# Optimization experiments

Measured on AMD Instinct MI355X. Metric: run time of the kernel, lower is better.

## Reference

```python
import jax, jax.numpy as jnp
import numpy as np

EPS = 1e-5
HEADS = 4
DIM_HEAD = 64


def setup_inputs() -> dict:
    key = jax.random.key(0)
    k1, k2, k3, k4, k5, k6 = jax.random.split(key, 6)
    B, C, T, H, W = 2, 128, 40, 8, 8
    inner = HEADS * DIM_HEAD  # 256
    x = jax.random.normal(k1, (B, C, T, H, W), dtype=jnp.float32)
    g = jnp.ones((1, C, 1, 1, 1), dtype=jnp.float32) + 0.1 * jax.random.normal(k2, (1, C, 1, 1, 1), dtype=jnp.float32)
    b = 0.1 * jax.random.normal(k3, (1, C, 1, 1, 1), dtype=jnp.float32)
    w_qkv = 0.02 * jax.random.normal(k4, (inner * 3, C), dtype=jnp.float32)  # Conv1d(dim, inner*3, 1) weight squeezed
    w_out = 0.02 * jax.random.normal(k5, (C, inner), dtype=jnp.float32)      # Conv1d(inner, dim, 1) weight squeezed
    b_out = 0.02 * jax.random.normal(k6, (C,), dtype=jnp.float32)
    return {"x": x, "g": g, "b": b, "w_qkv": w_qkv, "w_out": w_out, "b_out": b_out}


def reference(x, g, b, w_qkv, w_out, b_out):
    B, C, T, H, W = x.shape
    n = T * H * W
    scale = DIM_HEAD ** -0.5
    # channel LayerNorm (var over dim=1, unbiased=False)
    mean = jnp.mean(x, axis=1, keepdims=True)
    std = jnp.sqrt(jnp.var(x, axis=1, keepdims=True))
    xn = (x - mean) / (std + EPS) * g + b
    xf = xn.reshape(B, C, n)  # b c n
    # 1x1 conv == matmul over channels
    qkv = jnp.einsum('oc,bcn->bon', w_qkv, xf)
    q, k, v = jnp.split(qkv, 3, axis=1)  # each [B, heads*d, n]
    def to_heads(t):  # b (h d) n -> b h n d
        return t.reshape(B, HEADS, DIM_HEAD, n).transpose(0, 1, 3, 2)
    q, k, v = to_heads(q) * scale, to_heads(k), to_heads(v)
    sim = jnp.einsum('bhid,bhjd->bhij', q, k)
    attn = jax.nn.softmax(sim, axis=-1)
    out = jnp.einsum('bhij,bhjd->bhid', attn, v)
    out = out.transpose(0, 1, 3, 2).reshape(B, HEADS * DIM_HEAD, n)  # b (h d) n
    out = jnp.einsum('oc,bcn->bon', w_out, out) + b_out[None, :, None]
    return out.reshape(B, C, T, H, W)
```

## Files before the change

kernel.cpp:

```cpp
#include <hip/hip_runtime.h>
#include <hip/hip_bf16.h>

#define HEADS 4
#define DHEAD 64
#define CC 128
#define NPOS 2560
#define NB 2

#define XN_ELE  ((size_t)NB * NPOS * CC)
#define QKV_ELE ((size_t)NB * HEADS * NPOS * DHEAD)
#define WS_TOTAL (XN_ELE + 4 * QKV_ELE)

typedef __attribute__((ext_vector_type(8))) short short8;
typedef __attribute__((ext_vector_type(4))) short short4_t;
typedef __attribute__((ext_vector_type(4))) float f32x4;

#define SIDX(row, col) (((row) << 6) + ((col) ^ (((row) & 7) << 3)))

static __device__ __forceinline__ float b2f(short u) {
    union { unsigned int i; float f; } v;
    v.i = ((unsigned int)(unsigned short)u) << 16;
    return v.f;
}
static __device__ __forceinline__ short f2b(float f) {
    __hip_bfloat16 h = __float2bfloat16(f);
    union { __hip_bfloat16 h; unsigned short u; } v; v.h = h;
    return (short)v.u;
}

__global__ __launch_bounds__(256) void ln_kernel(
    const float* __restrict__ x, const float* __restrict__ g,
    const float* __restrict__ bb, short* __restrict__ xn) {
    int p0 = blockIdx.x * 64, b = blockIdx.y;
    __shared__ float tile[128][65];
    __shared__ float redsum[4][64], redsq[4][64], meanS[64], invS[64];
    int t = threadIdx.x, p = t & 63, cpart = t >> 6;
    float s = 0.f, sq = 0.f;
    for (int k = 0; k < 32; k++) {
        int c = cpart * 32 + k;
        float v = x[((b * CC + c) * NPOS) + p0 + p];
        tile[c][p] = v;
        s += v; sq += v * v;
    }
    redsum[cpart][p] = s; redsq[cpart][p] = sq;
    __syncthreads();
    if (t < 64) {
        float S = redsum[0][t] + redsum[1][t] + redsum[2][t] + redsum[3][t];
        float Q = redsq[0][t] + redsq[1][t] + redsq[2][t] + redsq[3][t];
        float mean = S * (1.f / CC);
        float var = fmaxf(Q * (1.f / CC) - mean * mean, 0.f);
        meanS[t] = mean;
        invS[t] = 1.f / (sqrtf(var) + 1e-5f);
    }
    __syncthreads();
    for (int k = 0; k < 32; k++) {
        int idx = k * 256 + t;
        int c = idx & 127, pp = idx >> 7;
        float v = (tile[c][pp] - meanS[pp]) * invS[pp] * g[c] + bb[c];
        xn[((size_t)(b * NPOS) + p0 + pp) * CC + c] = f2b(v);
    }
}

__global__ __launch_bounds__(256) void qkv_kernel(
    const float* __restrict__ w, const short* __restrict__ xn,
    short* __restrict__ q_ws, short* __restrict__ k_ws, short* __restrict__ v_ws) {
    int pt = blockIdx.x, ot = blockIdx.y, b = blockIdx.z;
    int p0 = pt * 64, o0 = ot * 64;
    __shared__ short Ws[64][136];
    __shared__ short Xs[64][136];
    int t = threadIdx.x, wv = t >> 6, l = t & 63;
    for (int i = 0; i < 8; i++) {
        int gidx = i * 256 + t;
        int r = gidx >> 5, cg = gidx & 31;
        f32x4 wv4 = *(const f32x4*)&w[(size_t)(o0 + r) * CC + cg * 4];
        short4_t sv = { f2b(wv4[0]), f2b(wv4[1]), f2b(wv4[2]), f2b(wv4[3]) };
        *(short4_t*)&Ws[r][cg * 4] = sv;
    }
    for (int i = 0; i < 4; i++) {
        int idx = i * 256 + t;
        int r = idx >> 4, ch = idx & 15;
        *(short8*)&Xs[r][ch * 8] = *(const short8*)&xn[((size_t)(b * NPOS) + p0 + r) * CC + ch * 8];
    }
    __syncthreads();
    f32x4 acc[4] = {{0,0,0,0},{0,0,0,0},{0,0,0,0},{0,0,0,0}};
    int lr = l & 15, lg = l >> 4;
    for (int kk = 0; kk < 4; kk++) {
        short8 a = *(short8*)&Ws[wv * 16 + lr][kk * 32 + lg * 8];
        for (int fb = 0; fb < 4; fb++) {
            short8 bf = *(short8*)&Xs[fb * 16 + lr][kk * 32 + lg * 8];
            acc[fb] = __builtin_amdgcn_mfma_f32_16x16x32_bf16(a, bf, acc[fb], 0, 0, 0);
        }
    }
    int orow0 = o0 + wv * 16 + lg * 4;
    int sec = orow0 >> 8;
    int oi = orow0 & 255, h = oi >> 6, d0 = oi & 63;
    size_t bh = (size_t)(b * HEADS + h);
    for (int fb = 0; fb < 4; fb++) {
        int pos = p0 + fb * 16 + lr;
        if (sec == 0) {
            short4_t qv = { f2b(acc[fb][0] * 0.125f), f2b(acc[fb][1] * 0.125f),
                            f2b(acc[fb][2] * 0.125f), f2b(acc[fb][3] * 0.125f) };
            *(short4_t*)&q_ws[(bh * NPOS + pos) * DHEAD + d0] = qv;
        } else if (sec == 1) {
            short4_t kv = { f2b(acc[fb][0]), f2b(acc[fb][1]), f2b(acc[fb][2]), f2b(acc[fb][3]) };
            *(short4_t*)&k_ws[(bh * NPOS + pos) * DHEAD + d0] = kv;
        } else {
            for (int r = 0; r < 4; r++)
                v_ws[(bh * DHEAD + d0 + r) * NPOS + pos] = f2b(acc[fb][r]);
        }
    }
}

__global__ __launch_bounds__(256) void attn_kernel(
    const short* __restrict__ q_ws, const short* __restrict__ k_ws,
    const short* __restrict__ v_ws, short* __restrict__ o_ws) {
    int qt = blockIdx.x, bh = blockIdx.y;
    int q0 = qt * 64;
    __shared__ short Ks[2][64 * 64];
    __shared__ short Vs[2][64 * 64];
    __shared__ short PsT[64 * 64];
    int t = threadIdx.x, wv = t >> 6, l = t & 63;
    int lr = l & 15, lg = l >> 4;
    int sr0 = t >> 3, sr1 = sr0 + 32, sc = (t & 7) * 8;
    const short* kbp = k_ws + (size_t)bh * NPOS * DHEAD;
    const short* vbp = v_ws + (size_t)bh * DHEAD * NPOS;

    short8 qreg[2];
    for (int kk = 0; kk < 2; kk++)
        qreg[kk] = *(const short8*)&q_ws[((size_t)bh * NPOS + q0 + wv * 16 + lr) * DHEAD + kk * 32 + lg * 8];

    *(short8*)&Ks[0][SIDX(sr0, sc)] = *(const short8*)&kbp[(size_t)sr0 * DHEAD + sc];
    *(short8*)&Ks[0][SIDX(sr1, sc)] = *(const short8*)&kbp[(size_t)sr1 * DHEAD + sc];
    *(short8*)&Vs[0][SIDX(sr0, sc)] = *(const short8*)&vbp[(size_t)sr0 * NPOS + sc];
    *(short8*)&Vs[0][SIDX(sr1, sc)] = *(const short8*)&vbp[(size_t)sr1 * NPOS + sc];
    __syncthreads();

    float m_ = -1e9f, l_ = 0.f;
    f32x4 acc[4] = {{0,0,0,0},{0,0,0,0},{0,0,0,0},{0,0,0,0}};
    int prow = wv * 16 + lr;

    for (int kt = 0; kt < NPOS / 64; kt++) {
        int cur = kt & 1;
        bool pf = (kt + 1 < NPOS / 64);
        short8 kr0, kr1, vr0, vr1;
        if (pf) {
            int koff = (kt + 1) * 64;
            kr0 = *(const short8*)&kbp[(size_t)(koff + sr0) * DHEAD + sc];
            kr1 = *(const short8*)&kbp[(size_t)(koff + sr1) * DHEAD + sc];
            vr0 = *(const short8*)&vbp[(size_t)sr0 * NPOS + koff + sc];
            vr1 = *(const short8*)&vbp[(size_t)sr1 * NPOS + koff + sc];
        }
        f32x4 sf[4] = {{0,0,0,0},{0,0,0,0},{0,0,0,0},{0,0,0,0}};
        #pragma unroll
        for (int kk = 0; kk < 2; kk++) {
            #pragma unroll
            for (int fb = 0; fb < 4; fb++) {
                short8 kb = *(short8*)&Ks[cur][SIDX(fb * 16 + lr, kk * 32 + lg * 8)];
                sf[fb] = __builtin_amdgcn_mfma_f32_16x16x32_bf16(kb, qreg[kk], sf[fb], 0, 0, 0);
            }
        }
        float m0 = fmaxf(fmaxf(sf[0][0], sf[0][1]), fmaxf(sf[0][2], sf[0][3]));
        float m1 = fmaxf(fmaxf(sf[1][0], sf[1][1]), fmaxf(sf[1][2], sf[1][3]));
        float m2 = fmaxf(fmaxf(sf[2][0], sf[2][1]), fmaxf(sf[2][2], sf[2][3]));
        float m3 = fmaxf(fmaxf(sf[3][0], sf[3][1]), fmaxf(sf[3][2], sf[3][3]));
        float mx = fmaxf(fmaxf(m0, m1), fmaxf(m2, m3));
        mx = fmaxf(mx, __shfl_xor(mx, 16, 64));
        mx = fmaxf(mx, __shfl_xor(mx, 32, 64));
        float nm = fmaxf(m_, mx);
        float alpha = __expf(m_ - nm);
        float ps[4][4];
        float rs = 0.f;
        #pragma unroll
        for (int fb = 0; fb < 4; fb++) {
            float s0 = __expf(sf[fb][0] - nm), s1 = __expf(sf[fb][1] - nm);
            float s2 = __expf(sf[fb][2] - nm), s3 = __expf(sf[fb][3] - nm);
            ps[fb][0] = s0; ps[fb][1] = s1; ps[fb][2] = s2; ps[fb][3] = s3;
            rs += (s0 + s1) + (s2 + s3);
        }
        rs += __shfl_xor(rs, 16, 64);
        rs += __shfl_xor(rs, 32, 64);
        l_ = l_ * alpha + rs;
        m_ = nm;
        #pragma unroll
        for (int db = 0; db < 4; db++) {
            acc[db][0] *= alpha; acc[db][1] *= alpha;
            acc[db][2] *= alpha; acc[db][3] *= alpha;
        }
        #pragma unroll
        for (int fb = 0; fb < 4; fb++) {
            short4_t pk = { f2b(ps[fb][0]), f2b(ps[fb][1]), f2b(ps[fb][2]), f2b(ps[fb][3]) };
            *(short4_t*)&PsT[SIDX(prow, fb * 16 + lg * 4)] = pk;
        }
        #pragma unroll
        for (int kk = 0; kk < 2; kk++) {
            short8 pb = *(short8*)&PsT[SIDX(prow, kk * 32 + lg * 8)];
            #pragma unroll
            for (int db = 0; db < 4; db++) {
                short8 va = *(short8*)&Vs[cur][SIDX(db * 16 + lr, kk * 32 + lg * 8)];
                acc[db] = __builtin_amdgcn_mfma_f32_16x16x32_bf16(va, pb, acc[db], 0, 0, 0);
            }
        }
        if (pf) {
            *(short8*)&Ks[cur ^ 1][SIDX(sr0, sc)] = kr0;
            *(short8*)&Ks[cur ^ 1][SIDX(sr1, sc)] = kr1;
            *(short8*)&Vs[cur ^ 1][SIDX(sr0, sc)] = vr0;
            *(short8*)&Vs[cur ^ 1][SIDX(sr1, sc)] = vr1;
        }
        __syncthreads();
    }

    int h = bh & (HEADS - 1), b = bh >> 2;
    float inv = 1.f / l_;
    int pos = q0 + prow;
    #pragma unroll
    for (int db = 0; db < 4; db++) {
        short4_t ov = { f2b(acc[db][0] * inv), f2b(acc[db][1] * inv),
                        f2b(acc[db][2] * inv), f2b(acc[db][3] * inv) };
        *(short4_t*)&o_ws[((size_t)(b * NPOS) + pos) * 256 + h * DHEAD + db * 16 + lg * 4] = ov;
    }
}

__global__ __launch_bounds__(256) void proj_kernel(
    const float* __restrict__ w_out, const float* __restrict__ b_out,
    const short* __restrict__ o_ws, float* __restrict__ out) {
    int pt = blockIdx.x, ct = blockIdx.y, b = blockIdx.z;
    int p0 = pt * 64, c0 = ct * 64;
    __shared__ short Ws[64][72];
    __shared__ short Os[64][72];
    int t = threadIdx.x, wv = t >> 6, l = t & 63;
    int lr = l & 15, lg = l >> 4;
    f32x4 acc[4] = {{0,0,0,0},{0,0,0,0},{0,0,0,0},{0,0,0,0}};
    for (int kc = 0; kc < 4; kc++) {
        __syncthreads();
        for (int i = 0; i < 4; i++) {
            int gidx = i * 256 + t;
            int r = gidx >> 4, cg = gidx & 15;
            f32x4 wv4 = *(const f32x4*)&w_out[(size_t)(c0 + r) * 256 + kc * 64 + cg * 4];
            short4_t sv = { f2b(wv4[0]), f2b(wv4[1]), f2b(wv4[2]), f2b(wv4[3]) };
            *(short4_t*)&Ws[r][cg * 4] = sv;
        }
        for (int i = 0; i < 2; i++) {
            int idx = i * 256 + t;
            int r = idx >> 3, ch = idx & 7;
            *(short8*)&Os[r][ch * 8] = *(const short8*)&o_ws[((size_t)(b * NPOS) + p0 + r) * 256 + kc * 64 + ch * 8];
        }
        __syncthreads();
        for (int kk = 0; kk < 2; kk++) {
            short8 a = *(short8*)&Ws[wv * 16 + lr][kk * 32 + lg * 8];
            for (int fb = 0; fb < 4; fb++) {
                short8 ob = *(short8*)&Os[fb * 16 + lr][kk * 32 + lg * 8];
                acc[fb] = __builtin_amdgcn_mfma_f32_16x16x32_bf16(a, ob, acc[fb], 0, 0, 0);
            }
        }
    }
    for (int r = 0; r < 4; r++) {
        int c = c0 + wv * 16 + lg * 4 + r;
        float bias = b_out[c];
        for (int fb = 0; fb < 4; fb++) {
            float vv = acc[fb][r] + bias;
            out[((size_t)(b * CC) + c) * NPOS + p0 + fb * 16 + lr] = vv;
        }
    }
}

extern "C" void kernel_launch(void* const* d_in, const int* in_sizes, int n_in,
                              void* d_out, int out_size, void* d_ws, size_t ws_size,
                              hipStream_t stream) {
    const float* x     = (const float*)d_in[0];
    const float* g     = (const float*)d_in[1];
    const float* b     = (const float*)d_in[2];
    const float* w_qkv = (const float*)d_in[3];
    const float* w_out = (const float*)d_in[4];
    const float* b_out = (const float*)d_in[5];
    float* out = (float*)d_out;

    const size_t out_bytes = (size_t)out_size * sizeof(float);
    const size_t ws_need   = WS_TOTAL * sizeof(short);

    {
        const int exp_sizes[6] = {655360, 128, 128, 98304, 32768, 128};
        int bad = -1;
        if (n_in != 6) bad = 15;
        else for (int i = 0; i < 6; i++) if (in_sizes[i] != exp_sizes[i]) { bad = i; break; }
        if (bad >= 0) { hipMemsetAsync(d_out, 0x50 | bad, out_bytes, stream); return; }
    }
    if (ws_size < ws_need) {
        int mb = (int)(ws_size >> 20); if (mb > 15) mb = 15;
        hipMemsetAsync(d_out, 0x40 | mb, out_bytes, stream);
        return;
    }

    short* xn   = (short*)d_ws;
    short* q_ws = xn + XN_ELE;
    short* k_ws = q_ws + QKV_ELE;
    short* v_ws = k_ws + QKV_ELE;
    short* o_ws = v_ws + QKV_ELE;

    (void)hipGetLastError();
    ln_kernel<<<dim3(NPOS / 64, NB), 256, 0, stream>>>(x, g, b, xn);
    qkv_kernel<<<dim3(NPOS / 64, 12, NB), 256, 0, stream>>>(w_qkv, xn, q_ws, k_ws, v_ws);
    attn_kernel<<<dim3(NPOS / 64, NB * HEADS), 256, 0, stream>>>(q_ws, k_ws, v_ws, o_ws);
    proj_kernel<<<dim3(NPOS / 64, 2, NB), 256, 0, stream>>>(w_out, b_out, o_ws, out);
    if (hipGetLastError() != hipSuccess) {
        hipMemsetAsync(d_out, 0xF0, out_bytes, stream);
    }
}
```

Measured before the change: 135.2 us.

## Split attention KV range across blocks with combine kernel; single-stage proj staging

Adds a split-K flash-attention path. Each (q-tile, head) now has 4 blocks, each covering a quarter of the key range and writing partial outputs plus running max and sum, and a new combine kernel merges them with softmax rescaling. This raises the grid from 320 to 1280 blocks so the many CUs on the device are better filled, at the cost of extra workspace traffic and a kernel launch. The projection kernel also loads the full 256-wide K slice into LDS once instead of looping over four chunks with syncs. The split path only runs when the workspace is large enough, so whether it is active depends on the harness.

New measurement: 129.7 us. 4.1% less time.

```diff
diff --git a/kernel.cpp b/kernel.cpp
--- a/kernel.cpp
+++ b/kernel.cpp
@@ -6,10 +6,14 @@
 #define CC 128
 #define NPOS 2560
 #define NB 2
+#define NSPLIT 4
+#define NT_SPLIT ((NPOS / 64) / NSPLIT)
 
 #define XN_ELE  ((size_t)NB * NPOS * CC)
 #define QKV_ELE ((size_t)NB * HEADS * NPOS * DHEAD)
-#define WS_TOTAL (XN_ELE + 4 * QKV_ELE)
+#define WS_BASE_BYTES  ((XN_ELE + 4 * QKV_ELE) * 2)
+#define WS_SPLIT_BYTES ((XN_ELE + (4 + NSPLIT) * QKV_ELE) * 2 \
+                        + (size_t)NSPLIT * NB * HEADS * NPOS * 8)
 
 typedef __attribute__((ext_vector_type(8))) short short8;
 typedef __attribute__((ext_vector_type(4))) short short4_t;
@@ -111,40 +115,34 @@
     }
 }
 
-__global__ __launch_bounds__(256) void attn_kernel(
-    const short* __restrict__ q_ws, const short* __restrict__ k_ws,
-    const short* __restrict__ v_ws, short* __restrict__ o_ws) {
-    int qt = blockIdx.x, bh = blockIdx.y;
-    int q0 = qt * 64;
-    __shared__ short Ks[2][64 * 64];
-    __shared__ short Vs[2][64 * 64];
-    __shared__ short PsT[64 * 64];
-    int t = threadIdx.x, wv = t >> 6, l = t & 63;
+template <int NT>
+static __device__ __forceinline__ void attn_core(
+    const short* __restrict__ kbp, const short* __restrict__ vbp,
+    const short8* qreg, int kt0,
+    short* Ks0, short* Ks1, short* Vs0, short* Vs1, short* PsT,
+    int t, float& m_, float& l_, f32x4* acc) {
+    int wv = t >> 6, l = t & 63;
     int lr = l & 15, lg = l >> 4;
     int sr0 = t >> 3, sr1 = sr0 + 32, sc = (t & 7) * 8;
-    const short* kbp = k_ws + (size_t)bh * NPOS * DHEAD;
-    const short* vbp = v_ws + (size_t)bh * DHEAD * NPOS;
-
-    short8 qreg[2];
-    for (int kk = 0; kk < 2; kk++)
-        qreg[kk] = *(const short8*)&q_ws[((size_t)bh * NPOS + q0 + wv * 16 + lr) * DHEAD + kk * 32 + lg * 8];
-
-    *(short8*)&Ks[0][SIDX(sr0, sc)] = *(const short8*)&kbp[(size_t)sr0 * DHEAD + sc];
-    *(short8*)&Ks[0][SIDX(sr1, sc)] = *(const short8*)&kbp[(size_t)sr1 * DHEAD + sc];
-    *(short8*)&Vs[0][SIDX(sr0, sc)] = *(const short8*)&vbp[(size_t)sr0 * NPOS + sc];
-    *(short8*)&Vs[0][SIDX(sr1, sc)] = *(const short8*)&vbp[(size_t)sr1 * NPOS + sc];
-    __syncthreads();
-
-    float m_ = -1e9f, l_ = 0.f;
-    f32x4 acc[4] = {{0,0,0,0},{0,0,0,0},{0,0,0,0},{0,0,0,0}};
     int prow = wv * 16 + lr;
-
-    for (int kt = 0; kt < NPOS / 64; kt++) {
-        int cur = kt & 1;
-        bool pf = (kt + 1 < NPOS / 64);
+    short* KsA[2] = { Ks0, Ks1 };
+    short* VsA[2] = { Vs0, Vs1 };
+
+    {
+        int koff = kt0 * 64;
+        *(short8*)&KsA[0][SIDX(sr0, sc)] = *(const short8*)&kbp[(size_t)(koff + sr0) * DHEAD + sc];
+        *(short8*)&KsA[0][SIDX(sr1, sc)] = *(const short8*)&kbp[(size_t)(koff + sr1) * DHEAD + sc];
+        *(short8*)&VsA[0][SIDX(sr0, sc)] = *(const short8*)&vbp[(size_t)sr0 * NPOS + koff + sc];
+        *(short8*)&VsA[0][SIDX(sr1, sc)] = *(const short8*)&vbp[(size_t)sr1 * NPOS + koff + sc];
+    }
+    __syncthreads();
+
+    for (int it = 0; it < NT; it++) {
+        int cur = it & 1;
+        bool pf = (it + 1 < NT);
         short8 kr0, kr1, vr0, vr1;
         if (pf) {
-            int koff = (kt + 1) * 64;
+            int koff = (kt0 + it + 1) * 64;
             kr0 = *(const short8*)&kbp[(size_t)(koff + sr0) * DHEAD + sc];
             kr1 = *(const short8*)&kbp[(size_t)(koff + sr1) * DHEAD + sc];
             vr0 = *(const short8*)&vbp[(size_t)sr0 * NPOS + koff + sc];
@@ -155,7 +153,7 @@
         for (int kk = 0; kk < 2; kk++) {
             #pragma unroll
             for (int fb = 0; fb < 4; fb++) {
-                short8 kb = *(short8*)&Ks[cur][SIDX(fb * 16 + lr, kk * 32 + lg * 8)];
+                short8 kb = *(short8*)&KsA[cur][SIDX(fb * 16 + lr, kk * 32 + lg * 8)];
                 sf[fb] = __builtin_amdgcn_mfma_f32_16x16x32_bf16(kb, qreg[kk], sf[fb], 0, 0, 0);
             }
         }
@@ -196,28 +194,114 @@
             short8 pb = *(short8*)&PsT[SIDX(prow, kk * 32 + lg * 8)];
             #pragma unroll
             for (int db = 0; db < 4; db++) {
-                short8 va = *(short8*)&Vs[cur][SIDX(db * 16 + lr, kk * 32 + lg * 8)];
+                short8 va = *(short8*)&VsA[cur][SIDX(db * 16 + lr, kk * 32 + lg * 8)];
                 acc[db] = __builtin_amdgcn_mfma_f32_16x16x32_bf16(va, pb, acc[db], 0, 0, 0);
             }
         }
         if (pf) {
-            *(short8*)&Ks[cur ^ 1][SIDX(sr0, sc)] = kr0;
-            *(short8*)&Ks[cur ^ 1][SIDX(sr1, sc)] = kr1;
-            *(short8*)&Vs[cur ^ 1][SIDX(sr0, sc)] = vr0;
-            *(short8*)&Vs[cur ^ 1][SIDX(sr1, sc)] = vr1;
+            *(short8*)&KsA[cur ^ 1][SIDX(sr0, sc)] = kr0;
+            *(short8*)&KsA[cur ^ 1][SIDX(sr1, sc)] = kr1;
+            *(short8*)&VsA[cur ^ 1][SIDX(sr0, sc)] = vr0;
+            *(short8*)&VsA[cur ^ 1][SIDX(sr1, sc)] = vr1;
         }
         __syncthreads();
     }
-
+}
+
+__global__ __launch_bounds__(256) void attn_kernel(
+    const short* __restrict__ q_ws, const short* __restrict__ k_ws,
+    const short* __restrict__ v_ws, short* __restrict__ o_ws) {
+    int qt = blockIdx.x, bh = blockIdx.y;
+    int q0 = qt * 64;
+    __shared__ short Ks[2][64 * 64];
+    __shared__ short Vs[2][64 * 64];
+    __shared__ short PsT[64 * 64];
+    int t = threadIdx.x, wv = t >> 6, l = t & 63;
+    int lr = l & 15, lg = l >> 4;
+    const short* kbp = k_ws + (size_t)bh * NPOS * DHEAD;
+    const short* vbp = v_ws + (size_t)bh * DHEAD * NPOS;
+    short8 qreg[2];
+    for (int kk = 0; kk < 2; kk++)
+        qreg[kk] = *(const short8*)&q_ws[((size_t)bh * NPOS + q0 + wv * 16 + lr) * DHEAD + kk * 32 + lg * 8];
+    float m_ = -1e9f, l_ = 0.f;
+    f32x4 acc[4] = {{0,0,0,0},{0,0,0,0},{0,0,0,0},{0,0,0,0}};
+    attn_core<NPOS / 64>(kbp, vbp, qreg, 0, Ks[0], Ks[1], Vs[0], Vs[1], PsT, t, m_, l_, acc);
     int h = bh & (HEADS - 1), b = bh >> 2;
     float inv = 1.f / l_;
-    int pos = q0 + prow;
+    int pos = q0 + wv * 16 + lr;
     #pragma unroll
     for (int db = 0; db < 4; db++) {
         short4_t ov = { f2b(acc[db][0] * inv), f2b(acc[db][1] * inv),
                         f2b(acc[db][2] * inv), f2b(acc[db][3] * inv) };
         *(short4_t*)&o_ws[((size_t)(b * NPOS) + pos) * 256 + h * DHEAD + db * 16 + lg * 4] = ov;
     }
+}
+
+__global__ __launch_bounds__(256) void attn_split_kernel(
+    const short* __restrict__ q_ws, const short* __restrict__ k_ws,
+    const short* __restrict__ v_ws, short* __restrict__ po, float* __restrict__ ml) {
+    int qt = blockIdx.x, bh = blockIdx.y, s = blockIdx.z;
+    int q0 = qt * 64;
+    __shared__ short Ks[2][64 * 64];
+    __shared__ short Vs[2][64 * 64];
+    __shared__ short PsT[64 * 64];
+    int t = threadIdx.x, wv = t >> 6, l = t & 63;
+    int lr = l & 15, lg = l >> 4;
+    const short* kbp = k_ws + (size_t)bh * NPOS * DHEAD;
+    const short* vbp = v_ws + (size_t)bh * DHEAD * NPOS;
+    short8 qreg[2];
+    for (int kk = 0; kk < 2; kk++)
+        qreg[kk] = *(const short8*)&q_ws[((size_t)bh * NPOS + q0 + wv * 16 + lr) * DHEAD + kk * 32 + lg * 8];
+    float m_ = -1e9f, l_ = 0.f;
+    f32x4 acc[4] = {{0,0,0,0},{0,0,0,0},{0,0,0,0},{0,0,0,0}};
+    attn_core<NT_SPLIT>(kbp, vbp, qreg, s * NT_SPLIT, Ks[0], Ks[1], Vs[0], Vs[1], PsT, t, m_, l_, acc);
+    float inv = 1.f / l_;
+    int pos = q0 + wv * 16 + lr;
+    size_t sb = (size_t)(s * NB * HEADS + bh);
+    #pragma unroll
+    for (int db = 0; db < 4; db++) {
+        short4_t ov = { f2b(acc[db][0] * inv), f2b(acc[db][1] * inv),
+                        f2b(acc[db][2] * inv), f2b(acc[db][3] * inv) };
+        *(short4_t*)&po[(sb * NPOS + pos) * DHEAD + db * 16 + lg * 4] = ov;
+    }
+    if (lg == 0) {
+        ml[2 * (sb * NPOS + pos) + 0] = m_;
+        ml[2 * (sb * NPOS + pos) + 1] = l_;
+    }
+}
+
+__global__ __launch_bounds__(256) void combine_kernel(
+    const short* __restrict__ po, const float* __restrict__ ml, short* __restrict__ o_ws) {
+    int tid = blockIdx.x * 256 + threadIdx.x;
+    int c8 = tid & 31;
+    int posb = tid >> 5;
+    int b = posb / NPOS, pos = posb - b * NPOS;
+    int h = c8 >> 3, d0 = (c8 & 7) * 8;
+    int bh = b * HEADS + h;
+    float ms[NSPLIT], ls[NSPLIT], m = -1e30f;
+    #pragma unroll
+    for (int s = 0; s < NSPLIT; s++) {
+        size_t sb = (size_t)(s * NB * HEADS + bh);
+        ms[s] = ml[2 * (sb * NPOS + pos) + 0];
+        ls[s] = ml[2 * (sb * NPOS + pos) + 1];
+        m = fmaxf(m, ms[s]);
+    }
+    float w[NSPLIT], wsum = 0.f;
+    #pragma unroll
+    for (int s = 0; s < NSPLIT; s++) { w[s] = ls[s] * __expf(ms[s] - m); wsum += w[s]; }
+    float o8[8] = {0,0,0,0,0,0,0,0};
+    #pragma unroll
+    for (int s = 0; s < NSPLIT; s++) {
+        size_t sb = (size_t)(s * NB * HEADS + bh);
+        short8 v = *(const short8*)&po[(sb * NPOS + pos) * DHEAD + d0];
+        #pragma unroll
+        for (int j = 0; j < 8; j++) o8[j] += w[s] * b2f(v[j]);
+    }
+    float inv = 1.f / wsum;
+    short8 ov;
+    #pragma unroll
+    for (int j = 0; j < 8; j++) ov[j] = f2b(o8[j] * inv);
+    *(short8*)&o_ws[((size_t)posb) * 256 + h * DHEAD + d0] = ov;
 }
 
 __global__ __launch_bounds__(256) void proj_kernel(
@@ -225,32 +309,30 @@
     const short* __restrict__ o_ws, float* __restrict__ out) {
     int pt = blockIdx.x, ct = blockIdx.y, b = blockIdx.z;
     int p0 = pt * 64, c0 = ct * 64;
-    __shared__ short Ws[64][72];
-    __shared__ short Os[64][72];
+    __shared__ short Ws[64][264];
+    __shared__ short Os[64][264];
     int t = threadIdx.x, wv = t >> 6, l = t & 63;
     int lr = l & 15, lg = l >> 4;
+    for (int i = 0; i < 16; i++) {
+        int gidx = i * 256 + t;
+        int r = gidx >> 6, cg = gidx & 63;
+        f32x4 wv4 = *(const f32x4*)&w_out[(size_t)(c0 + r) * 256 + cg * 4];
+        short4_t sv = { f2b(wv4[0]), f2b(wv4[1]), f2b(wv4[2]), f2b(wv4[3]) };
+        *(short4_t*)&Ws[r][cg * 4] = sv;
+    }
+    for (int i = 0; i < 8; i++) {
+        int gidx = i * 256 + t;
+        int r = gidx >> 5, ch = gidx & 31;
+        *(short8*)&Os[r][ch * 8] = *(const short8*)&o_ws[((size_t)(b * NPOS) + p0 + r) * 256 + ch * 8];
+    }
+    __syncthreads();
     f32x4 acc[4] = {{0,0,0,0},{0,0,0,0},{0,0,0,0},{0,0,0,0}};
-    for (int kc = 0; kc < 4; kc++) {
-        __syncthreads();
-        for (int i = 0; i < 4; i++) {
-            int gidx = i * 256 + t;
-            int r = gidx >> 4, cg = gidx & 15;
-            f32x4 wv4 = *(const f32x4*)&w_out[(size_t)(c0 + r) * 256 + kc * 64 + cg * 4];
-            short4_t sv = { f2b(wv4[0]), f2b(wv4[1]), f2b(wv4[2]), f2b(wv4[3]) };
-            *(short4_t*)&Ws[r][cg * 4] = sv;
-        }
-        for (int i = 0; i < 2; i++) {
-            int idx = i * 256 + t;
-            int r = idx >> 3, ch = idx & 7;
-            *(short8*)&Os[r][ch * 8] = *(const short8*)&o_ws[((size_t)(b * NPOS) + p0 + r) * 256 + kc * 64 + ch * 8];
-        }
-        __syncthreads();
-        for (int kk = 0; kk < 2; kk++) {
-            short8 a = *(short8*)&Ws[wv * 16 + lr][kk * 32 + lg * 8];
-            for (int fb = 0; fb < 4; fb++) {
-                short8 ob = *(short8*)&Os[fb * 16 + lr][kk * 32 + lg * 8];
-                acc[fb] = __builtin_amdgcn_mfma_f32_16x16x32_bf16(a, ob, acc[fb], 0, 0, 0);
-            }
+    for (int kc = 0; kc < 8; kc++) {
+        short8 a = *(short8*)&Ws[wv * 16 + lr][kc * 32 + lg * 8];
+        #pragma unroll
+        for (int fb = 0; fb < 4; fb++) {
+            short8 ob = *(short8*)&Os[fb * 16 + lr][kc * 32 + lg * 8];
+            acc[fb] = __builtin_amdgcn_mfma_f32_16x16x32_bf16(a, ob, acc[fb], 0, 0, 0);
         }
     }
     for (int r = 0; r < 4; r++) {
@@ -275,7 +357,6 @@
     float* out = (float*)d_out;
 
     const size_t out_bytes = (size_t)out_size * sizeof(float);
-    const size_t ws_need   = WS_TOTAL * sizeof(short);
 
     {
         const int exp_sizes[6] = {655360, 128, 128, 98304, 32768, 128};
@@ -284,7 +365,7 @@
         else for (int i = 0; i < 6; i++) if (in_sizes[i] != exp_sizes[i]) { bad = i; break; }
         if (bad >= 0) { hipMemsetAsync(d_out, 0x50 | bad, out_bytes, stream); return; }
     }
-    if (ws_size < ws_need) {
+    if (ws_size < WS_BASE_BYTES) {
         int mb = (int)(ws_size >> 20); if (mb > 15) mb = 15;
         hipMemsetAsync(d_out, 0x40 | mb, out_bytes, stream);
         return;
@@ -295,11 +376,20 @@
     short* k_ws = q_ws + QKV_ELE;
     short* v_ws = k_ws + QKV_ELE;
     short* o_ws = v_ws + QKV_ELE;
+    short* po   = o_ws + QKV_ELE;
+    float* ml   = (float*)(po + NSPLIT * QKV_ELE);
+
+    const bool use_split = (ws_size >= WS_SPLIT_BYTES);
 
     (void)hipGetLastError();
     ln_kernel<<<dim3(NPOS / 64, NB), 256, 0, stream>>>(x, g, b, xn);
     qkv_kernel<<<dim3(NPOS / 64, 12, NB), 256, 0, stream>>>(w_qkv, xn, q_ws, k_ws, v_ws);
-    attn_kernel<<<dim3(NPOS / 64, NB * HEADS), 256, 0, stream>>>(q_ws, k_ws, v_ws, o_ws);
+    if (use_split) {
+        attn_split_kernel<<<dim3(NPOS / 64, NB * HEADS, NSPLIT), 256, 0, stream>>>(q_ws, k_ws, v_ws, po, ml);
+        combine_kernel<<<dim3(NB * NPOS * 32 / 256), 256, 0, stream>>>(po, ml, o_ws);
+    } else {
+        attn_kernel<<<dim3(NPOS / 64, NB * HEADS), 256, 0, stream>>>(q_ws, k_ws, v_ws, o_ws);
+    }
     proj_kernel<<<dim3(NPOS / 64, 2, NB), 256, 0, stream>>>(w_out, b_out, o_ws, out);
     if (hipGetLastError() != hipSuccess) {
         hipMemsetAsync(d_out, 0xF0, out_bytes, stream);
```
